# Optimization experiments

Hardware: AMD Instinct MI355X
Metric: run time of the kernel (lower is better)

Reference implementation:

```python
import jax, jax.numpy as jnp
import numpy as np

B, S, N = 8, 64, 256
STATE, IN_F, OUT_F = 128, 64, 64
ALPHA = 0.2
NEG = -9e15


def setup_inputs() -> dict:
    key = jax.random.key(0)
    ks = jax.random.split(key, 12)
    d = {
        "hyper_inputs": jax.random.normal(ks[0], (B, S, STATE), jnp.float32),
        "inputs": jax.random.normal(ks[1], (B, S, N, IN_F), jnp.float32),
        "Adj": jax.random.randint(ks[2], (N, N), 0, 2, jnp.int32),
        # hyper_w: Linear(STATE,32) -> ReLU -> Linear(32, OUT_F*IN_F)
        "w1": jax.random.normal(ks[3], (STATE, 32), jnp.float32) * 0.08,
        "b1": jax.random.normal(ks[4], (32,), jnp.float32) * 0.01,
        "w2": jax.random.normal(ks[5], (32, OUT_F * IN_F), jnp.float32) * 0.08,
        "b2": jax.random.normal(ks[6], (OUT_F * IN_F,), jnp.float32) * 0.01,
        # hyper_a: Linear(STATE,32) -> ReLU -> Linear(32, 2*OUT_F)
        "aw1": jax.random.normal(ks[7], (STATE, 32), jnp.float32) * 0.08,
        "ab1": jax.random.normal(ks[8], (32,), jnp.float32) * 0.01,
        "aw2": jax.random.normal(ks[9], (32, 2 * OUT_F), jnp.float32) * 0.08,
        "ab2": jax.random.normal(ks[10], (2 * OUT_F,), jnp.float32) * 0.01,
    }
    return d


def _leaky(x):
    return jnp.where(x >= 0, x, ALPHA * x)


def reference(hyper_inputs, inputs, Adj, w1, b1, w2, b2, aw1, ab1, aw2, ab2):
    # hypernetwork-generated per-(b,s) weights
    hdn = jax.nn.relu(hyper_inputs @ w1 + b1)            # [B,S,32]
    W = jnp.abs(hdn @ w2 + b2).reshape(B, S, IN_F, OUT_F)
    hda = jax.nn.relu(hyper_inputs @ aw1 + ab1)
    a = jnp.abs(hda @ aw2 + ab2)                          # [B,S,2*OUT_F]

    h = jnp.einsum('bsni,bsio->bsno', inputs, W)          # [B,S,N,OUT_F]

    # decomposed GAT scores: e[b,s,i,j] = leakyrelu(h_i.a1 + h_j.a2)
    a1, a2 = a[..., :OUT_F], a[..., OUT_F:]
    e1 = jnp.einsum('bsno,bso->bsn', h, a1)               # source term
    e2 = jnp.einsum('bsno,bso->bsn', h, a2)               # target term
    e = _leaky(e1[..., :, None] + e2[..., None, :])       # [B,S,N,N]

    attention = jnp.where(Adj > 0, e, NEG)
    # NOTE: faithful to original: softmax over dim=1 (the S axis)
    attention = jax.nn.softmax(attention, axis=1)
    h_prime = jnp.einsum('bsij,bsjo->bsio', attention, h)  # [B,S,N,OUT_F]
    return jax.nn.elu(h_prime)                              # concat=True branch
```

## Files before the change

kernel.cpp:

```cpp
#include <hip/hip_runtime.h>
#include <hip/hip_bf16.h>
#include <math.h>

#define BB 8
#define SS 64
#define NN 256
#define ST 128
#define IF 64
#define OF 64
#define H1 32
#define ALPHA 0.2f
#define LOG2E 1.4426950408889634f

typedef short short8 __attribute__((ext_vector_type(8)));
typedef short short4_t __attribute__((ext_vector_type(4)));
typedef float f32x4 __attribute__((ext_vector_type(4)));
typedef unsigned short ushort_t;

static __device__ __forceinline__ ushort_t f2bf(float f) {
    __hip_bfloat16 h = __float2bfloat16(f);
    return *reinterpret_cast<ushort_t*>(&h);
}

__global__ __launch_bounds__(512) void k_hyper2(
    const float* __restrict__ hyper,
    const float* __restrict__ w1, const float* __restrict__ b1,
    const float* __restrict__ w2, const float* __restrict__ b2,
    const float* __restrict__ aw1, const float* __restrict__ ab1,
    const float* __restrict__ aw2, const float* __restrict__ ab2,
    float* __restrict__ Wd, float* __restrict__ Aa)
{
    const int t = threadIdx.x;
    const int bs0 = blockIdx.x * 2;
    __shared__ float hy[2][ST];
    __shared__ float hdn_s[2][H1];
    __shared__ float hda_s[2][H1];
    if (t < 2 * ST)
        hy[t >> 7][t & 127] = hyper[(size_t)bs0 * ST + t];
    __syncthreads();
    if (t < 64) {
        const int q = t >> 5, c = t & 31;
        float acc = b1[c];
#pragma unroll 4
        for (int k = 0; k < ST; ++k) acc = fmaf(hy[q][k], w1[k * H1 + c], acc);
        hdn_s[q][c] = fmaxf(acc, 0.f);
    } else if (t < 128) {
        const int tt = t - 64;
        const int q = tt >> 5, c = tt & 31;
        float acc = ab1[c];
#pragma unroll 4
        for (int k = 0; k < ST; ++k) acc = fmaf(hy[q][k], aw1[k * H1 + c], acc);
        hda_s[q][c] = fmaxf(acc, 0.f);
    }
    __syncthreads();
    if (t < 256) {
        const int q = t >> 7, c = t & 127;
        float a = ab2[c];
#pragma unroll
        for (int k = 0; k < H1; ++k)
            a = fmaf(hda_s[q][k], aw2[k * 128 + c], a);
        Aa[(size_t)(bs0 + q) * 128 + c] = fabsf(a);
    }
#pragma unroll
    for (int p = 0; p < 2; ++p) {
        const int e = t * 4 + p * 2048;
        const float4 bb = *(const float4*)&b2[e];
        float4 a0 = bb, a1 = bb;
#pragma unroll
        for (int kq = 0; kq < 8; ++kq) {
            const float4 h0 = *(const float4*)&hdn_s[0][kq * 4];
            const float4 h1 = *(const float4*)&hdn_s[1][kq * 4];
#pragma unroll
            for (int c = 0; c < 4; ++c) {
                const float4 wv = *(const float4*)&w2[(size_t)(kq * 4 + c) * 4096 + e];
                const float s0 = (c == 0) ? h0.x : (c == 1) ? h0.y : (c == 2) ? h0.z : h0.w;
                const float s1 = (c == 0) ? h1.x : (c == 1) ? h1.y : (c == 2) ? h1.z : h1.w;
                a0.x = fmaf(s0, wv.x, a0.x); a0.y = fmaf(s0, wv.y, a0.y);
                a0.z = fmaf(s0, wv.z, a0.z); a0.w = fmaf(s0, wv.w, a0.w);
                a1.x = fmaf(s1, wv.x, a1.x); a1.y = fmaf(s1, wv.y, a1.y);
                a1.z = fmaf(s1, wv.z, a1.z); a1.w = fmaf(s1, wv.w, a1.w);
            }
        }
        a0.x = fabsf(a0.x); a0.y = fabsf(a0.y); a0.z = fabsf(a0.z); a0.w = fabsf(a0.w);
        a1.x = fabsf(a1.x); a1.y = fabsf(a1.y); a1.z = fabsf(a1.z); a1.w = fabsf(a1.w);
        *(float4*)&Wd[(size_t)(bs0 + 0) * 4096 + e] = a0;
        *(float4*)&Wd[(size_t)(bs0 + 1) * 4096 + e] = a1;
    }
}

__global__ __launch_bounds__(256) void k_h(
    const float* __restrict__ x, const float* __restrict__ Wd,
    const float* __restrict__ Aa,
    ushort_t* __restrict__ HbTw, float* __restrict__ E1, float* __restrict__ E2)
{
    const int bs = blockIdx.x;
    const int tid = threadIdx.x;
    const int wid = tid >> 6;
    const int lane = tid & 63;
    const int l15 = lane & 15;
    const int lhi = lane >> 4;

    __shared__ ushort_t Wt[IF * OF];
    __shared__ float wa1s[IF], wa2s[IF];
    __shared__ float a1s[OF], a2s[OF];

    if (tid < 64) a1s[tid] = Aa[(size_t)bs * 128 + tid];
    else if (tid < 128) a2s[tid - 64] = Aa[(size_t)bs * 128 + tid];

    {
        const float4* w4 = (const float4*)(Wd + (size_t)bs * 4096);
#pragma unroll
        for (int p = 0; p < 4; ++p) {
            const int idx = tid + p * 256;
            const float4 f = w4[idx];
            const int k = (idx * 4) >> 6;
            const int o0 = (idx * 4) & 63;
            Wt[(o0 + 0) * 64 + (k ^ (((o0 + 0) & 7) << 3))] = f2bf(f.x);
            Wt[(o0 + 1) * 64 + (k ^ (((o0 + 1) & 7) << 3))] = f2bf(f.y);
            Wt[(o0 + 2) * 64 + (k ^ (((o0 + 2) & 7) << 3))] = f2bf(f.z);
            Wt[(o0 + 3) * 64 + (k ^ (((o0 + 3) & 7) << 3))] = f2bf(f.w);
        }
    }
    __syncthreads();

    if (tid < 64) {
        const float4* wr = (const float4*)(Wd + (size_t)bs * 4096 + tid * 64);
        float s1 = 0.f, s2 = 0.f;
#pragma unroll
        for (int q = 0; q < 16; ++q) {
            const float4 f = wr[q];
            const float4 u = *(const float4*)&a1s[q * 4];
            const float4 v = *(const float4*)&a2s[q * 4];
            s1 += f.x * u.x + f.y * u.y + f.z * u.z + f.w * u.w;
            s2 += f.x * v.x + f.y * v.y + f.z * v.z + f.w * v.w;
        }
        wa1s[tid] = s1; wa2s[tid] = s2;
    }
    __syncthreads();

    {
        const float4* xr = (const float4*)(x + ((size_t)bs * NN + tid) * IF);
        float s1 = 0.f, s2 = 0.f;
#pragma unroll
        for (int q = 0; q < 16; ++q) {
            const float4 f = xr[q];
            const float4 u = *(const float4*)&wa1s[q * 4];
            const float4 v = *(const float4*)&wa2s[q * 4];
            s1 += f.x * u.x + f.y * u.y + f.z * u.z + f.w * u.w;
            s2 += f.x * v.x + f.y * v.y + f.z * v.z + f.w * v.w;
        }
        E1[(size_t)bs * NN + tid] = s1 * LOG2E;
        E2[(size_t)bs * NN + tid] = s2 * LOG2E;
    }

    f32x4 acc[4][4];
#pragma unroll
    for (int mt = 0; mt < 4; ++mt)
#pragma unroll
        for (int nt = 0; nt < 4; ++nt) acc[mt][nt] = (f32x4){0.f, 0.f, 0.f, 0.f};

    short8 af[4][2];
#pragma unroll
    for (int mt = 0; mt < 4; ++mt) {
        const int row = wid * 64 + mt * 16 + l15;
        const float* xrow = x + ((size_t)bs * NN + row) * IF;
#pragma unroll
        for (int ks = 0; ks < 2; ++ks) {
            const int k0 = ks * 32 + lhi * 8;
            const float4 fa = *(const float4*)&xrow[k0];
            const float4 fb = *(const float4*)&xrow[k0 + 4];
            short8 pk;
            pk[0] = (short)f2bf(fa.x); pk[1] = (short)f2bf(fa.y);
            pk[2] = (short)f2bf(fa.z); pk[3] = (short)f2bf(fa.w);
            pk[4] = (short)f2bf(fb.x); pk[5] = (short)f2bf(fb.y);
            pk[6] = (short)f2bf(fb.z); pk[7] = (short)f2bf(fb.w);
            af[mt][ks] = pk;
        }
    }
    short8 bfr[4][2];
#pragma unroll
    for (int nt = 0; nt < 4; ++nt) {
        const int o = nt * 16 + l15;
#pragma unroll
        for (int ks = 0; ks < 2; ++ks) {
            const int k0 = ks * 32 + lhi * 8;
            bfr[nt][ks] = *(const short8*)&Wt[o * 64 + (k0 ^ ((o & 7) << 3))];
        }
    }
#pragma unroll
    for (int mt = 0; mt < 4; ++mt)
#pragma unroll
        for (int nt = 0; nt < 4; ++nt) {
            acc[mt][nt] = __builtin_amdgcn_mfma_f32_16x16x32_bf16(
                af[mt][0], bfr[nt][0], acc[mt][nt], 0, 0, 0);
            acc[mt][nt] = __builtin_amdgcn_mfma_f32_16x16x32_bf16(
                af[mt][1], bfr[nt][1], acc[mt][nt], 0, 0, 0);
        }

    ushort_t* hbw = HbTw + (size_t)bs * (OF * NN);
#pragma unroll
    for (int mt = 0; mt < 4; ++mt) {
        const int nb = wid * 8 + mt * 2 + (lhi >> 1);
        const int ne = (lhi & 1) * 4;
#pragma unroll
        for (int nt = 0; nt < 4; ++nt) {
            short4_t pk;
            pk[0] = (short)f2bf(acc[mt][nt][0]);
            pk[1] = (short)f2bf(acc[mt][nt][1]);
            pk[2] = (short)f2bf(acc[mt][nt][2]);
            pk[3] = (short)f2bf(acc[mt][nt][3]);
            *(short4_t*)(hbw + ((size_t)(nt * 32 + nb) * 16 + l15) * 8 + ne) = pk;
        }
    }
}

__global__ __launch_bounds__(256) void k_softstats(
    const float* __restrict__ E1, const float* __restrict__ E2,
    const int* __restrict__ Adj, unsigned int* __restrict__ MRw)
{
    const int bid = blockIdx.x;
    const int b = bid >> 6, i0 = (bid & 63) * 4;
    const int t = threadIdx.x;
    __shared__ float e1s[4][SS];
    {
        const int ii = t >> 6, s = t & 63;
        e1s[ii][s] = E1[(size_t)(b * SS + s) * NN + i0 + ii];
    }
    float e2r[SS];
#pragma unroll
    for (int s = 0; s < SS; ++s)
        e2r[s] = E2[(size_t)(b * SS + s) * NN + t];
    __syncthreads();

#pragma unroll
    for (int ii = 0; ii < 4; ++ii) {
        float v[SS];
        float mx = -3.0e38f;
#pragma unroll
        for (int s = 0; s < SS; ++s) {
            float u = e1s[ii][s] + e2r[s];
            u = fmaxf(u, ALPHA * u);
            v[s] = u;
            mx = fmaxf(mx, u);
        }
        const unsigned int mu = (unsigned int)f2bf(mx);
        const float mUse = __uint_as_float(mu << 16);
        float sum = 0.f;
#pragma unroll
        for (int s = 0; s < SS; ++s)
            sum += exp2f(v[s] - mUse);
        const int i = i0 + ii;
        const int adj = Adj[(size_t)i * NN + t];
        const float r = (adj > 0) ? (1.f / sum) : -0.015625f;
        MRw[((((size_t)b * 16 + (i >> 4)) * 32 + (t >> 3)) * 16 + (i & 15)) * 8
            + (t & 7)] = (mu << 16) | (unsigned int)f2bf(r);
    }
}

__global__ __launch_bounds__(512) void k_attn(
    const ushort_t* __restrict__ HbTw, const float* __restrict__ E1,
    const float* __restrict__ E2, const unsigned int* __restrict__ MRw,
    float* __restrict__ out)
{
    const int bs = blockIdx.x;
    const int b = bs >> 6;
    const int tid = threadIdx.x;
    const int wid = tid >> 6;
    const int lane = tid & 63;
    const int l15 = lane & 15;
    const int lhi = lane >> 4;

    __shared__ float e2s[NN];
    if (tid < NN) e2s[tid] = E2[(size_t)bs * NN + tid];
    __syncthreads();

    float e1r[2];
#pragma unroll
    for (int mt = 0; mt < 2; ++mt)
        e1r[mt] = E1[(size_t)bs * NN + wid * 32 + mt * 16 + l15];

    f32x4 acc[2][4];
#pragma unroll
    for (int mt = 0; mt < 2; ++mt)
#pragma unroll
        for (int nt = 0; nt < 4; ++nt) acc[mt][nt] = (f32x4){0.f, 0.f, 0.f, 0.f};

    const ushort_t* hbw = HbTw + (size_t)bs * (OF * NN);
    const unsigned int* mrb = MRw + (size_t)b * (NN * NN);
    const unsigned int* mr0 = mrb + ((size_t)(wid * 2 + 0) * 32) * 128 + l15 * 8;
    const unsigned int* mr1 = mrb + ((size_t)(wid * 2 + 1) * 32) * 128 + l15 * 8;

    for (int ch = 0; ch < 4; ++ch) {
        short8 bfr[4][2];
#pragma unroll
        for (int nt = 0; nt < 4; ++nt) {
#pragma unroll
            for (int ks = 0; ks < 2; ++ks) {
                const int nb = ch * 8 + ks * 4 + lhi;
                bfr[nt][ks] = *(const short8*)(hbw
                    + ((size_t)(nt * 32 + nb) * 16 + l15) * 8);
            }
        }
        uint4 mq[2][2][2];
#pragma unroll
        for (int ks = 0; ks < 2; ++ks) {
            const int kb = ch * 8 + ks * 4 + lhi;
            mq[0][ks][0] = *(const uint4*)(mr0 + kb * 128);
            mq[0][ks][1] = *(const uint4*)(mr0 + kb * 128 + 4);
            mq[1][ks][0] = *(const uint4*)(mr1 + kb * 128);
            mq[1][ks][1] = *(const uint4*)(mr1 + kb * 128 + 4);
        }
        float e2v[2][8];
#pragma unroll
        for (int ks = 0; ks < 2; ++ks) {
            const int k0 = ch * 64 + ks * 32 + lhi * 8;
            const float4 lo = *(const float4*)&e2s[k0];
            const float4 hi = *(const float4*)&e2s[k0 + 4];
            e2v[ks][0] = lo.x; e2v[ks][1] = lo.y; e2v[ks][2] = lo.z; e2v[ks][3] = lo.w;
            e2v[ks][4] = hi.x; e2v[ks][5] = hi.y; e2v[ks][6] = hi.z; e2v[ks][7] = hi.w;
        }
#pragma unroll
        for (int mt = 0; mt < 2; ++mt) {
            const float e1v = e1r[mt];
            short8 af[2];
#pragma unroll
            for (int ks = 0; ks < 2; ++ks) {
                const unsigned int wv[8] = {
                    mq[mt][ks][0].x, mq[mt][ks][0].y, mq[mt][ks][0].z, mq[mt][ks][0].w,
                    mq[mt][ks][1].x, mq[mt][ks][1].y, mq[mt][ks][1].z, mq[mt][ks][1].w};
                short8 pk;
#pragma unroll
                for (int kk = 0; kk < 8; ++kk) {
                    const float Mf = __uint_as_float(wv[kk] & 0xFFFF0000u);
                    const float Rf = __uint_as_float(wv[kk] << 16);
                    float v = e1v + e2v[ks][kk];
                    v = fmaxf(v, ALPHA * v);
                    const float a = (Rf < 0.f) ? -Rf : exp2f(v - Mf) * Rf;
                    pk[kk] = (short)f2bf(a);
                }
                af[ks] = pk;
            }
#pragma unroll
            for (int nt = 0; nt < 4; ++nt) {
                acc[mt][nt] = __builtin_amdgcn_mfma_f32_16x16x32_bf16(
                    af[0], bfr[nt][0], acc[mt][nt], 0, 0, 0);
                acc[mt][nt] = __builtin_amdgcn_mfma_f32_16x16x32_bf16(
                    af[1], bfr[nt][1], acc[mt][nt], 0, 0, 0);
            }
        }
    }

    float* ob = out + (size_t)bs * (NN * OF);
#pragma unroll
    for (int mt = 0; mt < 2; ++mt) {
        const int rbase = wid * 32 + mt * 16 + lhi * 4;
#pragma unroll
        for (int nt = 0; nt < 4; ++nt) {
            const int o = nt * 16 + l15;
#pragma unroll
            for (int reg = 0; reg < 4; ++reg) {
                float v = acc[mt][nt][reg];
                v = (v > 0.f) ? v : (__expf(v) - 1.f);
                ob[(size_t)(rbase + reg) * OF + o] = v;
            }
        }
    }
}

extern "C" void kernel_launch(void* const* d_in, const int* in_sizes, int n_in,
                              void* d_out, int out_size, void* d_ws, size_t ws_size,
                              hipStream_t stream)
{
    const float* hyper = (const float*)d_in[0];
    const float* x     = (const float*)d_in[1];
    const int*   Adj   = (const int*)d_in[2];
    const float* w1    = (const float*)d_in[3];
    const float* b1    = (const float*)d_in[4];
    const float* w2    = (const float*)d_in[5];
    const float* b2    = (const float*)d_in[6];
    const float* aw1   = (const float*)d_in[7];
    const float* ab1   = (const float*)d_in[8];
    const float* aw2   = (const float*)d_in[9];
    const float* ab2   = (const float*)d_in[10];
    float* out = (float*)d_out;

    float* ws      = (float*)d_ws;
    float* Wd      = ws;
    float* Aa      = Wd + 2097152;
    ushort_t* HbTw = (ushort_t*)(Aa + 65536);
    float* E1      = (float*)(HbTw + 8388608);
    float* E2      = E1 + 131072;
    unsigned int* MRw = (unsigned int*)(E2 + 131072);

    k_hyper2<<<dim3(256), dim3(512), 0, stream>>>(hyper, w1, b1, w2, b2,
                                                  aw1, ab1, aw2, ab2, Wd, Aa);
    k_h<<<dim3(512), dim3(256), 0, stream>>>(x, Wd, Aa, HbTw, E1, E2);
    k_softstats<<<dim3(512), dim3(256), 0, stream>>>(E1, E2, Adj, MRw);
    k_attn<<<dim3(512), dim3(512), 0, stream>>>(HbTw, E1, E2, MRw, out);
}
```

Measured before the change: 75.23 us.

## Stage x in swizzled LDS, split attention blocks in half, interleave batch order

k_h now copies the whole 64KB input tile into XOR-swizzled shared memory once and reads it from there, instead of loading each row from global memory twice. k_attn is split into twice as many 256-thread blocks, each covering half the rows, with launch bounds allowing four blocks per CU. Its inner loop is restructured per k-step to shrink live registers. Block indexing in k_softstats and k_attn now interleaves the batch index, probably to spread the MRw/Adj working sets across caches. The 64KB LDS buffer limits k_h occupancy, and each split attn block reloads the same H and E2 data.

Result: faster. 73.24 us, median of 2 (-2.6%).

```diff
diff --git a/kernel.cpp b/kernel.cpp
--- a/kernel.cpp
+++ b/kernel.cpp
@@ -100,6 +100,7 @@
     const int l15 = lane & 15;
     const int lhi = lane >> 4;
 
+    __shared__ char xl[NN * IF * 4];
     __shared__ ushort_t Wt[IF * OF];
     __shared__ float wa1s[IF], wa2s[IF];
     __shared__ float a1s[OF], a2s[OF];
@@ -107,6 +108,16 @@
     if (tid < 64) a1s[tid] = Aa[(size_t)bs * 128 + tid];
     else if (tid < 128) a2s[tid - 64] = Aa[(size_t)bs * 128 + tid];
 
+    {
+        const float4* x4 = (const float4*)(x + (size_t)bs * NN * IF);
+#pragma unroll
+        for (int p = 0; p < 16; ++p) {
+            const int idx = tid + p * 256;
+            const int row = idx >> 4;
+            const int byte = (row << 8) | ((((idx & 15) << 4)) ^ ((row & 7) << 5));
+            *(float4*)(xl + byte) = x4[idx];
+        }
+    }
     {
         const float4* w4 = (const float4*)(Wd + (size_t)bs * 4096);
 #pragma unroll
@@ -139,11 +150,12 @@
     __syncthreads();
 
     {
-        const float4* xr = (const float4*)(x + ((size_t)bs * NN + tid) * IF);
         float s1 = 0.f, s2 = 0.f;
+        const int rbase = tid << 8;
+        const int sw = (tid & 7) << 5;
 #pragma unroll
         for (int q = 0; q < 16; ++q) {
-            const float4 f = xr[q];
+            const float4 f = *(const float4*)(xl + (rbase | ((q << 4) ^ sw)));
             const float4 u = *(const float4*)&wa1s[q * 4];
             const float4 v = *(const float4*)&wa2s[q * 4];
             s1 += f.x * u.x + f.y * u.y + f.z * u.z + f.w * u.w;
@@ -163,12 +175,13 @@
 #pragma unroll
     for (int mt = 0; mt < 4; ++mt) {
         const int row = wid * 64 + mt * 16 + l15;
-        const float* xrow = x + ((size_t)bs * NN + row) * IF;
+        const int rb = row << 8;
+        const int sw = (row & 7) << 5;
 #pragma unroll
         for (int ks = 0; ks < 2; ++ks) {
-            const int k0 = ks * 32 + lhi * 8;
-            const float4 fa = *(const float4*)&xrow[k0];
-            const float4 fb = *(const float4*)&xrow[k0 + 4];
+            const int kb = (ks * 32 + lhi * 8) * 4;
+            const float4 fa = *(const float4*)(xl + (rb | (kb ^ sw)));
+            const float4 fb = *(const float4*)(xl + (rb | ((kb + 16) ^ sw)));
             short8 pk;
             pk[0] = (short)f2bf(fa.x); pk[1] = (short)f2bf(fa.y);
             pk[2] = (short)f2bf(fa.z); pk[3] = (short)f2bf(fa.w);
@@ -218,8 +231,8 @@
     const float* __restrict__ E1, const float* __restrict__ E2,
     const int* __restrict__ Adj, unsigned int* __restrict__ MRw)
 {
-    const int bid = blockIdx.x;
-    const int b = bid >> 6, i0 = (bid & 63) * 4;
+    const int b = blockIdx.x & 7;
+    const int i0 = (blockIdx.x >> 3) * 4;
     const int t = threadIdx.x;
     __shared__ float e1s[4][SS];
     {
@@ -257,27 +270,31 @@
     }
 }
 
-__global__ __launch_bounds__(512) void k_attn(
+__global__ __launch_bounds__(256, 4) void k_attn(
     const ushort_t* __restrict__ HbTw, const float* __restrict__ E1,
     const float* __restrict__ E2, const unsigned int* __restrict__ MRw,
     float* __restrict__ out)
 {
-    const int bs = blockIdx.x;
-    const int b = bs >> 6;
+    const int b = blockIdx.x & 7;
+    const int k2 = blockIdx.x >> 3;
+    const int s = k2 >> 1;
+    const int half = k2 & 1;
+    const int bs = b * 64 + s;
     const int tid = threadIdx.x;
     const int wid = tid >> 6;
     const int lane = tid & 63;
     const int l15 = lane & 15;
     const int lhi = lane >> 4;
+    const int rb0 = half * 128 + wid * 32;
 
     __shared__ float e2s[NN];
-    if (tid < NN) e2s[tid] = E2[(size_t)bs * NN + tid];
+    e2s[tid] = E2[(size_t)bs * NN + tid];
     __syncthreads();
 
     float e1r[2];
 #pragma unroll
     for (int mt = 0; mt < 2; ++mt)
-        e1r[mt] = E1[(size_t)bs * NN + wid * 32 + mt * 16 + l15];
+        e1r[mt] = E1[(size_t)bs * NN + rb0 + mt * 16 + l15];
 
     f32x4 acc[2][4];
 #pragma unroll
@@ -287,73 +304,54 @@
 
     const ushort_t* hbw = HbTw + (size_t)bs * (OF * NN);
     const unsigned int* mrb = MRw + (size_t)b * (NN * NN);
-    const unsigned int* mr0 = mrb + ((size_t)(wid * 2 + 0) * 32) * 128 + l15 * 8;
-    const unsigned int* mr1 = mrb + ((size_t)(wid * 2 + 1) * 32) * 128 + l15 * 8;
+    const unsigned int* mr0 = mrb + ((size_t)((rb0 >> 4) + 0) * 32) * 128 + l15 * 8;
+    const unsigned int* mr1 = mrb + ((size_t)((rb0 >> 4) + 1) * 32) * 128 + l15 * 8;
 
     for (int ch = 0; ch < 4; ++ch) {
-        short8 bfr[4][2];
-#pragma unroll
-        for (int nt = 0; nt < 4; ++nt) {
-#pragma unroll
-            for (int ks = 0; ks < 2; ++ks) {
-                const int nb = ch * 8 + ks * 4 + lhi;
-                bfr[nt][ks] = *(const short8*)(hbw
-                    + ((size_t)(nt * 32 + nb) * 16 + l15) * 8);
-            }
-        }
-        uint4 mq[2][2][2];
 #pragma unroll
         for (int ks = 0; ks < 2; ++ks) {
             const int kb = ch * 8 + ks * 4 + lhi;
-            mq[0][ks][0] = *(const uint4*)(mr0 + kb * 128);
-            mq[0][ks][1] = *(const uint4*)(mr0 + kb * 128 + 4);
-            mq[1][ks][0] = *(const uint4*)(mr1 + kb * 128);
-            mq[1][ks][1] = *(const uint4*)(mr1 + kb * 128 + 4);
-        }
-        float e2v[2][8];
-#pragma unroll
-        for (int ks = 0; ks < 2; ++ks) {
+            short8 bfr[4];
+#pragma unroll
+            for (int nt = 0; nt < 4; ++nt)
+                bfr[nt] = *(const short8*)(hbw + ((size_t)(nt * 32 + kb) * 16 + l15) * 8);
+            uint4 mq[2][2];
+            mq[0][0] = *(const uint4*)(mr0 + kb * 128);
+            mq[0][1] = *(const uint4*)(mr0 + kb * 128 + 4);
+            mq[1][0] = *(const uint4*)(mr1 + kb * 128);
+            mq[1][1] = *(const uint4*)(mr1 + kb * 128 + 4);
             const int k0 = ch * 64 + ks * 32 + lhi * 8;
             const float4 lo = *(const float4*)&e2s[k0];
             const float4 hi = *(const float4*)&e2s[k0 + 4];
-            e2v[ks][0] = lo.x; e2v[ks][1] = lo.y; e2v[ks][2] = lo.z; e2v[ks][3] = lo.w;
-            e2v[ks][4] = hi.x; e2v[ks][5] = hi.y; e2v[ks][6] = hi.z; e2v[ks][7] = hi.w;
-        }
-#pragma unroll
-        for (int mt = 0; mt < 2; ++mt) {
-            const float e1v = e1r[mt];
-            short8 af[2];
-#pragma unroll
-            for (int ks = 0; ks < 2; ++ks) {
+            const float e2v[8] = {lo.x, lo.y, lo.z, lo.w, hi.x, hi.y, hi.z, hi.w};
+#pragma unroll
+            for (int mt = 0; mt < 2; ++mt) {
+                const float e1v = e1r[mt];
                 const unsigned int wv[8] = {
-                    mq[mt][ks][0].x, mq[mt][ks][0].y, mq[mt][ks][0].z, mq[mt][ks][0].w,
-                    mq[mt][ks][1].x, mq[mt][ks][1].y, mq[mt][ks][1].z, mq[mt][ks][1].w};
+                    mq[mt][0].x, mq[mt][0].y, mq[mt][0].z, mq[mt][0].w,
+                    mq[mt][1].x, mq[mt][1].y, mq[mt][1].z, mq[mt][1].w};
                 short8 pk;
 #pragma unroll
                 for (int kk = 0; kk < 8; ++kk) {
                     const float Mf = __uint_as_float(wv[kk] & 0xFFFF0000u);
                     const float Rf = __uint_as_float(wv[kk] << 16);
-                    float v = e1v + e2v[ks][kk];
+                    float v = e1v + e2v[kk];
                     v = fmaxf(v, ALPHA * v);
                     const float a = (Rf < 0.f) ? -Rf : exp2f(v - Mf) * Rf;
                     pk[kk] = (short)f2bf(a);
                 }
-                af[ks] = pk;
+#pragma unroll
+                for (int nt = 0; nt < 4; ++nt)
+                    acc[mt][nt] = __builtin_amdgcn_mfma_f32_16x16x32_bf16(
+                        pk, bfr[nt], acc[mt][nt], 0, 0, 0);
             }
-#pragma unroll
-            for (int nt = 0; nt < 4; ++nt) {
-                acc[mt][nt] = __builtin_amdgcn_mfma_f32_16x16x32_bf16(
-                    af[0], bfr[nt][0], acc[mt][nt], 0, 0, 0);
-                acc[mt][nt] = __builtin_amdgcn_mfma_f32_16x16x32_bf16(
-                    af[1], bfr[nt][1], acc[mt][nt], 0, 0, 0);
-            }
         }
     }
 
     float* ob = out + (size_t)bs * (NN * OF);
 #pragma unroll
     for (int mt = 0; mt < 2; ++mt) {
-        const int rbase = wid * 32 + mt * 16 + lhi * 4;
+        const int rbase = rb0 + mt * 16 + lhi * 4;
 #pragma unroll
         for (int nt = 0; nt < 4; ++nt) {
             const int o = nt * 16 + l15;
@@ -396,5 +394,5 @@
                                                   aw1, ab1, aw2, ab2, Wd, Aa);
     k_h<<<dim3(512), dim3(256), 0, stream>>>(x, Wd, Aa, HbTw, E1, E2);
     k_softstats<<<dim3(512), dim3(256), 0, stream>>>(E1, E2, Adj, MRw);
-    k_attn<<<dim3(512), dim3(512), 0, stream>>>(HbTw, E1, E2, MRw, out);
-}
+    k_attn<<<dim3(1024), dim3(256), 0, stream>>>(HbTw, E1, E2, MRw, out);
+}
```
